# Kernel tuning notes

Measured on AMD Instinct MI355X. Metric: run time of the kernel, lower is better.

## Reference

```python
import jax, jax.numpy as jnp
import numpy as np


def setup_inputs() -> dict:
    key = jax.random.key(0)
    ks = jax.random.split(key, 8)
    B, L, K = 32, 1024, 256
    s = lambda k, shape, sc: jax.random.normal(k, shape, dtype=jnp.float32) * sc
    return {
        "x": s(ks[0], (B, L, K), 1.0),
        "rWx": s(ks[1], (K, 4 * K), 0.05),   # reader LSTM kernel
        "rWh": s(ks[2], (K, 4 * K), 0.05),   # reader recurrent kernel
        "rb": jnp.zeros((4 * K,), jnp.float32),
        "wWx": s(ks[3], (2 * K, 4 * K), 0.05),  # writer LSTM kernel (input dim 2K)
        "wWh": s(ks[4], (K, 4 * K), 0.05),
        "wb": jnp.zeros((4 * K,), jnp.float32),
        "cW": s(ks[5], (2 * K, 2 * K), 0.05),    # composer Dense(2K), linear activation
        "cb": jnp.zeros((2 * K,), jnp.float32),
    }


def _lstm(x_t, h, c, Wx, Wh, b):
    # Keras LSTM: gate order i, f, g(candidate), o; sigmoid recurrent activation, tanh activation
    gates = x_t @ Wx + h @ Wh + b
    i, f, g, o = jnp.split(gates, 4, axis=-1)
    c_new = jax.nn.sigmoid(f) * c + jax.nn.sigmoid(i) * jnp.tanh(g)
    h_new = jax.nn.sigmoid(o) * jnp.tanh(c_new)
    return h_new, c_new


def reference(x, rWx, rWh, rb, wWx, wWh, wb, cW, cb):
    B, L, K = x.shape
    zeros = jnp.zeros((B, K), x.dtype)
    # mem_0 = input (get_initial_state copies input to mem_0); LSTM states start at zero
    carry0 = (zeros, zeros, x, zeros, zeros)  # (hr, cr, mem, hw, cw)

    def step(carry, x_t):
        hr, cr, mem, hw, cw = carry
        # Eq 1: reader LSTM -> o_t
        hr, cr = _lstm(x_t, hr, cr, rWx, rWh, rb)  # o_t = hr, (B, K)
        # Eq 2-3: attention over memory
        z_t = jax.nn.softmax(jnp.einsum('bk,blk->bl', hr, mem), axis=-1)  # (B, L)
        m_rt = jnp.einsum('bl,blk->bk', z_t, mem)                          # (B, K)
        # Eq 4: composer (linear Dense on concat)
        c_t = jnp.concatenate([hr, m_rt], axis=-1) @ cW + cb               # (B, 2K)
        # Eq 5: writer LSTM -> h_t
        hw, cw = _lstm(c_t, hw, cw, wWx, wWh, wb)                          # (B, K)
        # Eq 6: memory update (selective forget + add)
        mem = mem * (1.0 - z_t[..., None]) + hw[:, None, :] * z_t[..., None]
        return (hr, cr, mem, hw, cw), hw

    _, hs = jax.lax.scan(step, carry0, jnp.swapaxes(x, 0, 1))
    # return_mode='all_outputs': full sequence of writer outputs
    return jnp.swapaxes(hs, 0, 1)  # (B, L, K)
```

## Files before the change

kernel.cpp:

```cpp
#include <hip/hip_runtime.h>
#include <math.h>


#define Bb 32
#define LL 1024
#define KK 256
#define ASCOPE __HIP_MEMORY_SCOPE_AGENT
#define FSTR 16

__device__ __forceinline__ float sigf(float v) { return 1.0f / (1.0f + __expf(-v)); }

__device__ __forceinline__ void st_coh2(float* p, float a, float b) {
    float2 v = make_float2(a, b);
    __hip_atomic_store((unsigned long long*)p,
                       __builtin_bit_cast(unsigned long long, v),
                       __ATOMIC_RELAXED, ASCOPE);
}
__device__ __forceinline__ float2 ld_coh2(const float* p) {
    unsigned long long u = __hip_atomic_load((const unsigned long long*)p,
                                             __ATOMIC_RELAXED, ASCOPE);
    return __builtin_bit_cast(float2, u);
}

__device__ __forceinline__ void bar_arrive(unsigned* fown, unsigned val) {
    asm volatile("s_waitcnt vmcnt(0) lgkmcnt(0)" ::: "memory");
    __syncthreads();
    if (threadIdx.x == 0)
        __hip_atomic_store(fown, val, __ATOMIC_RELAXED, ASCOPE);
}
__device__ __forceinline__ void bar_wait(unsigned* fbase, unsigned val) {
    if (threadIdx.x < 64) {
        for (;;) {
            unsigned v = __hip_atomic_load(fbase + threadIdx.x * FSTR,
                                           __ATOMIC_RELAXED, ASCOPE);
            if (__all(v >= val)) break;
            __builtin_amdgcn_s_sleep(1);
        }
    }
    asm volatile("" ::: "memory");
    __syncthreads();
}

__global__ __launch_bounds__(256) void k_pre(
    const float* __restrict__ cW, const float* __restrict__ cb,
    const float* __restrict__ wWx, const float* __restrict__ wb,
    const float* __restrict__ rWx, const float* __restrict__ rWh,
    const float* __restrict__ wWh,
    float* __restrict__ WfT, float* __restrict__ rWT, float* __restrict__ bfv,
    unsigned* __restrict__ flg) {
    int bid = blockIdx.x, tid = threadIdx.x;
    if (bid < 512) {
        __shared__ float srow[512];
        srow[tid] = cW[(size_t)bid * 512 + tid];
        srow[256 + tid] = cW[(size_t)bid * 512 + 256 + tid];
        __syncthreads();
#pragma unroll
        for (int rep = 0; rep < 4; rep++) {
            int col = rep * 256 + tid;
            float a = 0.f;
#pragma unroll 4
            for (int c = 0; c < 512; c++) a += srow[c] * wWx[(size_t)c * 1024 + col];
            WfT[(size_t)col * 768 + bid] = a;
        }
    } else if (bid < 516) {
        int col = (bid - 512) * 256 + tid;
        float a = wb[col];
#pragma unroll 4
        for (int c = 0; c < 512; c++) a += cb[c] * wWx[(size_t)c * 1024 + col];
        bfv[col] = a;
    } else if (bid < 644) {
        int k0 = (bid - 516) * 2;
        for (int kk = k0; kk < k0 + 2; kk++)
            for (int col = tid; col < 1024; col += 256)
                rWT[(size_t)col * 512 + kk] = rWx[(size_t)kk * 1024 + col];
    } else if (bid < 772) {
        int k0 = (bid - 644) * 2;
        for (int kk = k0; kk < k0 + 2; kk++)
            for (int col = tid; col < 1024; col += 256)
                rWT[(size_t)col * 512 + 256 + kk] = rWh[(size_t)kk * 1024 + col];
    } else if (bid < 900) {
        int k0 = (bid - 772) * 2;
        for (int kk = k0; kk < k0 + 2; kk++)
            for (int col = tid; col < 1024; col += 256)
                WfT[(size_t)col * 768 + 512 + kk] = wWh[(size_t)kk * 1024 + col];
    } else {
        int idx = (bid - 900) * 256 + tid;
        flg[idx] = 0u;
    }
}

__global__ __launch_bounds__(512, 1) void k_nse(
    const float* __restrict__ x, const float* __restrict__ rb,
    const float* __restrict__ rWT, const float* __restrict__ WfT,
    const float* __restrict__ bfv, float* __restrict__ st,
    float* __restrict__ out, unsigned* __restrict__ flg) {
    __shared__ float smem[32768 + 6144 + 160];
    float* memT   = smem;
    float* arena  = smem + 32768;
    float* sMw    = smem + 32768 + 6144;
    float* sSw    = sMw + 8;
    float* sMS    = sSw + 8;
    float* sScore = sMS + 16;

    float* hrb[2] = { st, st + 8192 };
    float* hwb[2] = { st + 16384, st + 24576 };
    float* partMS = st + 32832;
    float* partV  = st + 33344;

    int g = blockIdx.x, tid = threadIdx.x;
    int w = tid >> 6, ln = tid & 63;
    int bA = g >> 3;
    int bg = g >> 6, gl = g & 63;
    int j0 = gl * 4;
    int wstar = gl >> 3;
    unsigned* fA = flg + (bg * 64) * FSTR;
    unsigned* fB = flg + (256 + bg * 64) * FSTR;
    unsigned* fAo = fA + gl * FSTR;
    unsigned* fBo = fB + gl * FSTR;

    int ks = ln & 3, jq = (ln >> 2) & 3, gate = ln >> 4;
    int col = gate * KK + j0 + jq;
    int jl = ln & 3;
    int bw = bg * 8 + w;
    float* shb = arena + w * 768;
    float* sT  = arena + w * 640;

    const float4* wfc = (const float4*)(WfT + (size_t)col * 768);
    const float4* rwc = (const float4*)(rWT + (size_t)col * 512);
    float4 w2[16];
#pragma unroll
    for (int i = 0; i < 16; i++) w2[i] = wfc[64 + i * 4 + ks];
    float4 rw1[8];
#pragma unroll
    for (int i = 0; i < 8; i++) rw1[i] = rwc[i * 4 + ks];

    float crreg = 0.f, cwreg = 0.f;

    const float4* xsrc = (const float4*)(x + ((size_t)bA * LL + (size_t)(g & 7) * 128) * KK);
#pragma unroll
    for (int i = 0; i < 16; i++) ((float4*)memT)[tid + i * 512] = xsrc[tid + i * 512];
    {
        ((float4*)shb)[ln] = ((const float4*)(x + (size_t)bw * LL * KK))[ln];
        ((float4*)(shb + 256))[ln] = make_float4(0.f, 0.f, 0.f, 0.f);
        float racc = (ks == 0) ? rb[col] : 0.f;
        const float4* ip = (const float4*)shb;
#pragma unroll
        for (int i = 0; i < 8; i++) {
            float4 a = ip[i * 4 + ks];
            racc += a.x * rw1[i].x + a.y * rw1[i].y + a.z * rw1[i].z + a.w * rw1[i].w;
        }
#pragma unroll 8
        for (int i = 8; i < 32; i++) {
            int idx = i * 4 + ks;
            float4 a = ip[idx], q = rwc[idx];
            racc += a.x * q.x + a.y * q.y + a.z * q.z + a.w * q.w;
        }
        racc += __shfl_xor(racc, 1);
        racc += __shfl_xor(racc, 2);
        float gi = __shfl(racc, 4 * jl), gG = __shfl(racc, 32 + 4 * jl);
        float go = __shfl(racc, 48 + 4 * jl);
        float cn = sigf(gi) * tanhf(gG);
        float hn = sigf(go) * tanhf(cn);
        crreg = cn;
        float pa = __shfl(hn, 2 * (ln & 31)), pb = __shfl(hn, 2 * (ln & 31) + 1);
        if (ln < 2) st_coh2(hrb[0] + bw * KK + j0 + 2 * ln, pa, pb);
    }
    bar_arrive(fBo, 1u);
    float4 xreg = ((const float4*)(x + ((size_t)bw * LL + 1) * KK))[ln];
    bar_wait(fB, 1u);

    for (int t = 0; t < LL; t++) {
        int cur = t & 1, prv = cur ^ 1;
        const float* hp = hrb[cur] + bA * KK + ln * 4;
        float2 ha = ld_coh2(hp), hc = ld_coh2(hp + 2);
        float4 h4 = make_float4(ha.x, ha.y, hc.x, hc.y);
        float4 hrs2, hws2, w4 = make_float4(0.f, 0.f, 0.f, 0.f);
        {
            const float* hq = hrb[cur] + bw * KK + ln * 4;
            float2 a = ld_coh2(hq), c = ld_coh2(hq + 2);
            hrs2 = make_float4(a.x, a.y, c.x, c.y);
        }
        float Mprev = 0.f, invS = 0.f;
        if (t > 0) {
            const float* wp0 = hwb[prv] + bA * KK + ln * 4;
            float2 wa = ld_coh2(wp0), wc = ld_coh2(wp0 + 2);
            w4 = make_float4(wa.x, wa.y, wc.x, wc.y);
            const float* hq = hwb[prv] + bw * KK + ln * 4;
            float2 a = ld_coh2(hq), c = ld_coh2(hq + 2);
            hws2 = make_float4(a.x, a.y, c.x, c.y);
            Mprev = sMS[wstar * 2];
            invS = 1.0f / sMS[wstar * 2 + 1];
        } else {
            hws2 = make_float4(0.f, 0.f, 0.f, 0.f);
        }
        float dp[16];
        float* rowp = memT + w * 16 * KK;
        if (t > 0) {
            float scs[16];
            {
                const float4* sp = (const float4*)(sScore + w * 16);
#pragma unroll
                for (int q2 = 0; q2 < 4; q2++) {
                    float4 s4 = sp[q2];
                    scs[q2 * 4 + 0] = s4.x; scs[q2 * 4 + 1] = s4.y;
                    scs[q2 * 4 + 2] = s4.z; scs[q2 * 4 + 3] = s4.w;
                }
            }
#pragma unroll
            for (int i = 0; i < 16; i++) {
                float4* vp = (float4*)(rowp + i * KK) + ln;
                float4 v = *vp;
                float z = __expf(scs[i] - Mprev) * invS;
                float om = 1.0f - z;
                v.x = v.x * om + w4.x * z;
                v.y = v.y * om + w4.y * z;
                v.z = v.z * om + w4.z * z;
                v.w = v.w * om + w4.w * z;
                *vp = v;
                dp[i] = h4.x * v.x + h4.y * v.y + h4.z * v.z + h4.w * v.w;
            }
        } else {
#pragma unroll
            for (int i = 0; i < 16; i++) {
                float4 v = *((float4*)(rowp + i * KK) + ln);
                dp[i] = h4.x * v.x + h4.y * v.y + h4.z * v.z + h4.w * v.w;
            }
        }
        {
            int rr = ln >> 3, kk2 = ln & 7;
#pragma unroll
            for (int hh = 0; hh < 2; hh++) {
                int o = hh * 8;
                *(float2*)(sT + ln * 10 + 0) = make_float2(dp[o + 0], dp[o + 1]);
                *(float2*)(sT + ln * 10 + 2) = make_float2(dp[o + 2], dp[o + 3]);
                *(float2*)(sT + ln * 10 + 4) = make_float2(dp[o + 4], dp[o + 5]);
                *(float2*)(sT + ln * 10 + 6) = make_float2(dp[o + 6], dp[o + 7]);
                float ps = 0.f;
#pragma unroll
                for (int j = 0; j < 8; j++) ps += sT[(j * 8 + kk2) * 10 + rr];
                ps += __shfl_xor(ps, 1);
                ps += __shfl_xor(ps, 2);
                ps += __shfl_xor(ps, 4);
                if (kk2 == 0) sScore[w * 16 + o + rr] = ps;
            }
        }
        {
            float scs2[16];
            const float4* sp = (const float4*)(sScore + w * 16);
#pragma unroll
            for (int q2 = 0; q2 < 4; q2++) {
                float4 s4 = sp[q2];
                scs2[q2 * 4 + 0] = s4.x; scs2[q2 * 4 + 1] = s4.y;
                scs2[q2 * 4 + 2] = s4.z; scs2[q2 * 4 + 3] = s4.w;
            }
            float M16 = scs2[0];
#pragma unroll
            for (int i = 1; i < 16; i++) M16 = fmaxf(M16, scs2[i]);
            float Sw = 0.f;
            float4 Vw = make_float4(0.f, 0.f, 0.f, 0.f);
#pragma unroll
            for (int i = 0; i < 16; i++) {
                float e = __expf(scs2[i] - M16);
                Sw += e;
                float4 v = *((float4*)(rowp + i * KK) + ln);
                Vw.x += e * v.x; Vw.y += e * v.y; Vw.z += e * v.z; Vw.w += e * v.w;
            }
            ((float4*)(arena + w * 640))[ln] = Vw;
            if (ln == 0) { sMw[w] = M16; sSw[w] = Sw; }
        }
        __syncthreads();
        if (tid < 128) {
            float M = sMw[0];
#pragma unroll
            for (int q2 = 1; q2 < 8; q2++) M = fmaxf(M, sMw[q2]);
            float S = 0.f, V0 = 0.f, V1 = 0.f;
#pragma unroll
            for (int q2 = 0; q2 < 8; q2++) {
                float e = __expf(sMw[q2] - M);
                S += e * sSw[q2];
                V0 += e * arena[q2 * 640 + 2 * tid];
                V1 += e * arena[q2 * 640 + 2 * tid + 1];
            }
            st_coh2(partV + (size_t)g * KK + 2 * tid, V0, V1);
            if (tid == 0) st_coh2(partMS + g * 2, M, S);
        }
        bar_arrive(fAo, (unsigned)(t + 1));

        if (t + 1 < LL) ((float4*)shb)[ln] = xreg;
        ((float4*)(shb + 256))[ln] = hrs2;
        ((float4*)(shb + 512))[ln] = hws2;

        {
            unsigned tgt = (unsigned)(t + 1);
            for (;;) {
                unsigned v = tgt;
                if (ln < 8)
                    v = __hip_atomic_load(fA + (8 * w + ln) * FSTR, __ATOMIC_RELAXED, ASCOPE);
                if (__all(v >= tgt)) break;
                __builtin_amdgcn_s_sleep(1);
            }
        }
        float2 pms[8], pva[8], pvb[8];
#pragma unroll
        for (int q2 = 0; q2 < 8; q2++) {
            pms[q2] = ld_coh2(partMS + (bw * 8 + q2) * 2);
            const float* pv = partV + (size_t)(bw * 8 + q2) * KK + ln * 4;
            pva[q2] = ld_coh2(pv);
            pvb[q2] = ld_coh2(pv + 2);
        }
        float gpre;
        {
            float acc = (ks == 0) ? bfv[col] : 0.f;
            const float4* ip1 = (const float4*)(shb + 256);
            const float4* ip2 = (const float4*)(shb + 512);
#pragma unroll 8
            for (int i = 0; i < 16; i++) {
                int idx = i * 4 + ks;
                float4 a = ip1[idx], q = wfc[idx];
                acc += a.x * q.x + a.y * q.y + a.z * q.z + a.w * q.w;
            }
#pragma unroll 8
            for (int i = 0; i < 16; i++) {
                int idx = i * 4 + ks;
                float4 a = ip2[idx], q = wfc[128 + idx];
                acc += a.x * q.x + a.y * q.y + a.z * q.z + a.w * q.w;
            }
            gpre = acc;
        }
        if (t + 1 < LL) {
            float racc = (ks == 0) ? rb[col] : 0.f;
            const float4* ip = (const float4*)shb;
#pragma unroll
            for (int i = 0; i < 8; i++) {
                float4 a = ip[i * 4 + ks];
                racc += a.x * rw1[i].x + a.y * rw1[i].y + a.z * rw1[i].z + a.w * rw1[i].w;
            }
#pragma unroll 8
            for (int i = 8; i < 32; i++) {
                int idx = i * 4 + ks;
                float4 a = ip[idx], q = rwc[idx];
                racc += a.x * q.x + a.y * q.y + a.z * q.z + a.w * q.w;
            }
            racc += __shfl_xor(racc, 1);
            racc += __shfl_xor(racc, 2);
            float gi = __shfl(racc, 4 * jl), gf = __shfl(racc, 16 + 4 * jl);
            float gG = __shfl(racc, 32 + 4 * jl), go = __shfl(racc, 48 + 4 * jl);
            float cn = sigf(gf) * crreg + sigf(gi) * tanhf(gG);
            float hn = sigf(go) * tanhf(cn);
            crreg = cn;
            float pa = __shfl(hn, 2 * (ln & 31)), pb = __shfl(hn, 2 * (ln & 31) + 1);
            if (ln < 2) st_coh2(hrb[prv] + bw * KK + j0 + 2 * ln, pa, pb);
        }
        {
            float M = pms[0].x;
#pragma unroll
            for (int q2 = 1; q2 < 8; q2++) M = fmaxf(M, pms[q2].x);
            float S = 0.f;
            float4 V = make_float4(0.f, 0.f, 0.f, 0.f);
#pragma unroll
            for (int q2 = 0; q2 < 8; q2++) {
                float e = __expf(pms[q2].x - M);
                S += e * pms[q2].y;
                V.x += e * pva[q2].x; V.y += e * pva[q2].y;
                V.z += e * pvb[q2].x; V.w += e * pvb[q2].y;
            }
            float rS = 1.0f / S;
            ((float4*)shb)[ln] = make_float4(V.x * rS, V.y * rS, V.z * rS, V.w * rS);
            if (ln == 0) { sMS[w * 2] = M; sMS[w * 2 + 1] = S; }
            float acc = gpre;
            const float4* ip = (const float4*)shb;
#pragma unroll
            for (int i = 0; i < 16; i++) {
                float4 a = ip[i * 4 + ks];
                acc += a.x * w2[i].x + a.y * w2[i].y + a.z * w2[i].z + a.w * w2[i].w;
            }
            acc += __shfl_xor(acc, 1);
            acc += __shfl_xor(acc, 2);
            float gi = __shfl(acc, 4 * jl), gf = __shfl(acc, 16 + 4 * jl);
            float gG = __shfl(acc, 32 + 4 * jl), go = __shfl(acc, 48 + 4 * jl);
            float cp = (t > 0) ? cwreg : 0.f;
            float cn = sigf(gf) * cp + sigf(gi) * tanhf(gG);
            float hn = sigf(go) * tanhf(cn);
            cwreg = cn;
            float pa = __shfl(hn, 2 * (ln & 31)), pb = __shfl(hn, 2 * (ln & 31) + 1);
            if (ln < 2) {
                st_coh2(hwb[cur] + bw * KK + j0 + 2 * ln, pa, pb);
                *(float2*)(out + ((size_t)bw * LL + t) * KK + j0 + 2 * ln) =
                    make_float2(pa, pb);
            }
        }
        bar_arrive(fBo, (unsigned)(t + 2));
        if (t + 2 < LL)
            xreg = ((const float4*)(x + ((size_t)bw * LL + (size_t)(t + 2)) * KK))[ln];
        bar_wait(fB, (unsigned)(t + 2));
    }
}

extern "C" void kernel_launch(void* const* d_in, const int* in_sizes, int n_in,
                              void* d_out, int out_size, void* d_ws, size_t ws_size,
                              hipStream_t stream) {
    const float* x   = (const float*)d_in[0];
    const float* rWx = (const float*)d_in[1];
    const float* rWh = (const float*)d_in[2];
    const float* rb  = (const float*)d_in[3];
    const float* wWx = (const float*)d_in[4];
    const float* wWh = (const float*)d_in[5];
    const float* wb  = (const float*)d_in[6];
    const float* cW  = (const float*)d_in[7];
    const float* cb  = (const float*)d_in[8];
    float* out = (float*)d_out;

    float* ws = (float*)d_ws;
    float* WfT = ws;
    float* rWT = ws + 786432;
    float* bfv = ws + 786432 + 524288;
    float* st  = bfv + 1024;
    unsigned* flg = (unsigned*)(st + 98880);

    k_pre<<<932, 256, 0, stream>>>(cW, cb, wWx, wb, rWx, rWh, wWh, WfT, rWT, bfv, flg);

    const float* a_x = x; const float* a_rb = rb;
    const float* a_rWT = rWT; const float* a_WfT = WfT; const float* a_bf = bfv;
    float* a_st = st; float* a_out = out; unsigned* a_flg = flg;
    void* args[] = { &a_x, &a_rb, &a_rWT, &a_WfT, &a_bf, &a_st, &a_out, &a_flg };
    hipLaunchCooperativeKernel(reinterpret_cast<void*>(k_nse), dim3(256), dim3(512),
                               args, 0, stream);
}
```

Measured before the change: 15.01 ms.

## Share LSTM gate weights across batch rows by re-partitioning gate GEMV work

Before, each wavefront computed all 16 gate columns for one batch row, so every wave re-read the same weight columns. Now each wavefront owns two gate columns and computes them for all 8 batch rows of the group, reading inputs from a block-wide shared arena. Partial sums go through shared memory, and 32 threads then apply the LSTM cell nonlinearities. This cuts redundant weight traffic and register pressure (the rw1 cache is dropped), at the cost of extra __syncthreads per step. The arena stride is padded to 776 and the transpose scratch stride to 9, with staggered read offsets, to reduce LDS bank conflicts.

```diff
diff --git a/kernel.cpp b/kernel.cpp
--- a/kernel.cpp
+++ b/kernel.cpp
@@ -5,6 +5,7 @@
 #define Bb 32
 #define LL 1024
 #define KK 256
+#define AR 776
 #define ASCOPE __HIP_MEMORY_SCOPE_AGENT
 #define FSTR 16
 
@@ -94,13 +95,15 @@
     const float* __restrict__ rWT, const float* __restrict__ WfT,
     const float* __restrict__ bfv, float* __restrict__ st,
     float* __restrict__ out, unsigned* __restrict__ flg) {
-    __shared__ float smem[32768 + 6144 + 160];
+    __shared__ float smem[32768 + 8 * AR + 8 + 8 + 16 + 128 + 128 + 128];
     float* memT   = smem;
     float* arena  = smem + 32768;
-    float* sMw    = smem + 32768 + 6144;
+    float* sMw    = arena + 8 * AR;
     float* sSw    = sMw + 8;
     float* sMS    = sSw + 8;
     float* sScore = sMS + 16;
+    float* sGr    = sScore + 128;
+    float* sGw    = sGr + 128;
 
     float* hrb[2] = { st, st + 8192 };
     float* hwb[2] = { st + 16384, st + 24576 };
@@ -112,61 +115,58 @@
     int bA = g >> 3;
     int bg = g >> 6, gl = g & 63;
     int j0 = gl * 4;
-    int wstar = gl >> 3;
     unsigned* fA = flg + (bg * 64) * FSTR;
     unsigned* fB = flg + (256 + bg * 64) * FSTR;
     unsigned* fAo = fA + gl * FSTR;
     unsigned* fBo = fB + gl * FSTR;
 
-    int ks = ln & 3, jq = (ln >> 2) & 3, gate = ln >> 4;
-    int col = gate * KK + j0 + jq;
-    int jl = ln & 3;
-    int bw = bg * 8 + w;
-    float* shb = arena + w * 768;
-    float* sT  = arena + w * 640;
+    int bln = ln & 7, ks = (ln >> 3) & 3, cp = ln >> 5;
+    int c = 2 * w + cp;
+    int gate = c >> 2, jlc = c & 3;
+    int col = gate * KK + j0 + jlc;
+    int bglw = bg * 8 + w;
 
     const float4* wfc = (const float4*)(WfT + (size_t)col * 768);
     const float4* rwc = (const float4*)(rWT + (size_t)col * 512);
     float4 w2[16];
 #pragma unroll
-    for (int i = 0; i < 16; i++) w2[i] = wfc[64 + i * 4 + ks];
-    float4 rw1[8];
-#pragma unroll
-    for (int i = 0; i < 8; i++) rw1[i] = rwc[i * 4 + ks];
+    for (int i = 0; i < 16; i++) w2[i] = wfc[64 + ks * 16 + ((i + 3 * ks) & 15)];
 
     float crreg = 0.f, cwreg = 0.f;
 
     const float4* xsrc = (const float4*)(x + ((size_t)bA * LL + (size_t)(g & 7) * 128) * KK);
 #pragma unroll
     for (int i = 0; i < 16; i++) ((float4*)memT)[tid + i * 512] = xsrc[tid + i * 512];
+    ((float4*)(arena + w * AR))[ln] = ((const float4*)(x + (size_t)bglw * LL * KK))[ln];
+    ((float4*)(arena + w * AR + 256))[ln] = make_float4(0.f, 0.f, 0.f, 0.f);
+    __syncthreads();
     {
-        ((float4*)shb)[ln] = ((const float4*)(x + (size_t)bw * LL * KK))[ln];
-        ((float4*)(shb + 256))[ln] = make_float4(0.f, 0.f, 0.f, 0.f);
-        float racc = (ks == 0) ? rb[col] : 0.f;
-        const float4* ip = (const float4*)shb;
-#pragma unroll
-        for (int i = 0; i < 8; i++) {
-            float4 a = ip[i * 4 + ks];
-            racc += a.x * rw1[i].x + a.y * rw1[i].y + a.z * rw1[i].z + a.w * rw1[i].w;
-        }
+        float accr = 0.f;
+        const float4* ain = (const float4*)(arena + bln * AR);
 #pragma unroll 8
-        for (int i = 8; i < 32; i++) {
-            int idx = i * 4 + ks;
-            float4 a = ip[idx], q = rwc[idx];
-            racc += a.x * q.x + a.y * q.y + a.z * q.z + a.w * q.w;
-        }
-        racc += __shfl_xor(racc, 1);
-        racc += __shfl_xor(racc, 2);
-        float gi = __shfl(racc, 4 * jl), gG = __shfl(racc, 32 + 4 * jl);
-        float go = __shfl(racc, 48 + 4 * jl);
+        for (int i = 0; i < 32; i++) {
+            int idx = ks * 32 + ((i + 5 * ks) & 31);
+            float4 a = ain[idx], q = rwc[idx];
+            accr += a.x * q.x + a.y * q.y + a.z * q.z + a.w * q.w;
+        }
+        accr += __shfl_xor(accr, 8);
+        accr += __shfl_xor(accr, 16);
+        if (!(ln & 24)) sGr[c * 8 + bln] = accr + rb[col];
+    }
+    __syncthreads();
+    if (tid < 32) {
+        int pb = tid & 7, pj = tid >> 3;
+        int bgp = bg * 8 + pb;
+        float gi = sGr[(0 + pj) * 8 + pb], gG = sGr[(8 + pj) * 8 + pb];
+        float go = sGr[(12 + pj) * 8 + pb];
         float cn = sigf(gi) * tanhf(gG);
         float hn = sigf(go) * tanhf(cn);
         crreg = cn;
-        float pa = __shfl(hn, 2 * (ln & 31)), pb = __shfl(hn, 2 * (ln & 31) + 1);
-        if (ln < 2) st_coh2(hrb[0] + bw * KK + j0 + 2 * ln, pa, pb);
+        float hn2 = __shfl(hn, tid + 8);
+        if (!(pj & 1)) st_coh2(hrb[0] + bgp * KK + j0 + pj, hn, hn2);
     }
     bar_arrive(fBo, 1u);
-    float4 xreg = ((const float4*)(x + ((size_t)bw * LL + 1) * KK))[ln];
+    float4 xreg = ((const float4*)(x + ((size_t)bglw * LL + 1) * KK))[ln];
     bar_wait(fB, 1u);
 
     for (int t = 0; t < LL; t++) {
@@ -176,20 +176,20 @@
         float4 h4 = make_float4(ha.x, ha.y, hc.x, hc.y);
         float4 hrs2, hws2, w4 = make_float4(0.f, 0.f, 0.f, 0.f);
         {
-            const float* hq = hrb[cur] + bw * KK + ln * 4;
-            float2 a = ld_coh2(hq), c = ld_coh2(hq + 2);
-            hrs2 = make_float4(a.x, a.y, c.x, c.y);
+            const float* hq = hrb[cur] + bglw * KK + ln * 4;
+            float2 a = ld_coh2(hq), cc = ld_coh2(hq + 2);
+            hrs2 = make_float4(a.x, a.y, cc.x, cc.y);
         }
         float Mprev = 0.f, invS = 0.f;
         if (t > 0) {
             const float* wp0 = hwb[prv] + bA * KK + ln * 4;
             float2 wa = ld_coh2(wp0), wc = ld_coh2(wp0 + 2);
             w4 = make_float4(wa.x, wa.y, wc.x, wc.y);
-            const float* hq = hwb[prv] + bw * KK + ln * 4;
-            float2 a = ld_coh2(hq), c = ld_coh2(hq + 2);
-            hws2 = make_float4(a.x, a.y, c.x, c.y);
-            Mprev = sMS[wstar * 2];
-            invS = 1.0f / sMS[wstar * 2 + 1];
+            const float* hq = hwb[prv] + bglw * KK + ln * 4;
+            float2 a = ld_coh2(hq), cc = ld_coh2(hq + 2);
+            hws2 = make_float4(a.x, a.y, cc.x, cc.y);
+            Mprev = sMS[(bA & 7) * 2];
+            invS = 1.0f / sMS[(bA & 7) * 2 + 1];
         } else {
             hws2 = make_float4(0.f, 0.f, 0.f, 0.f);
         }
@@ -197,14 +197,12 @@
         float* rowp = memT + w * 16 * KK;
         if (t > 0) {
             float scs[16];
-            {
-                const float4* sp = (const float4*)(sScore + w * 16);
-#pragma unroll
-                for (int q2 = 0; q2 < 4; q2++) {
-                    float4 s4 = sp[q2];
-                    scs[q2 * 4 + 0] = s4.x; scs[q2 * 4 + 1] = s4.y;
-                    scs[q2 * 4 + 2] = s4.z; scs[q2 * 4 + 3] = s4.w;
-                }
+            const float4* sp = (const float4*)(sScore + w * 16);
+#pragma unroll
+            for (int q2 = 0; q2 < 4; q2++) {
+                float4 s4 = sp[q2];
+                scs[q2 * 4 + 0] = s4.x; scs[q2 * 4 + 1] = s4.y;
+                scs[q2 * 4 + 2] = s4.z; scs[q2 * 4 + 3] = s4.w;
             }
 #pragma unroll
             for (int i = 0; i < 16; i++) {
@@ -227,17 +225,16 @@
             }
         }
         {
+            float* sT = arena + w * AR;
             int rr = ln >> 3, kk2 = ln & 7;
 #pragma unroll
             for (int hh = 0; hh < 2; hh++) {
                 int o = hh * 8;
-                *(float2*)(sT + ln * 10 + 0) = make_float2(dp[o + 0], dp[o + 1]);
-                *(float2*)(sT + ln * 10 + 2) = make_float2(dp[o + 2], dp[o + 3]);
-                *(float2*)(sT + ln * 10 + 4) = make_float2(dp[o + 4], dp[o + 5]);
-                *(float2*)(sT + ln * 10 + 6) = make_float2(dp[o + 6], dp[o + 7]);
+#pragma unroll
+                for (int j = 0; j < 8; j++) sT[ln * 9 + j] = dp[o + j];
                 float ps = 0.f;
 #pragma unroll
-                for (int j = 0; j < 8; j++) ps += sT[(j * 8 + kk2) * 10 + rr];
+                for (int j = 0; j < 8; j++) ps += sT[(j * 8 + kk2) * 9 + rr];
                 ps += __shfl_xor(ps, 1);
                 ps += __shfl_xor(ps, 2);
                 ps += __shfl_xor(ps, 4);
@@ -265,7 +262,7 @@
                 float4 v = *((float4*)(rowp + i * KK) + ln);
                 Vw.x += e * v.x; Vw.y += e * v.y; Vw.z += e * v.z; Vw.w += e * v.w;
             }
-            ((float4*)(arena + w * 640))[ln] = Vw;
+            ((float4*)(arena + w * AR))[ln] = Vw;
             if (ln == 0) { sMw[w] = M16; sSw[w] = Sw; }
         }
         __syncthreads();
@@ -278,17 +275,49 @@
             for (int q2 = 0; q2 < 8; q2++) {
                 float e = __expf(sMw[q2] - M);
                 S += e * sSw[q2];
-                V0 += e * arena[q2 * 640 + 2 * tid];
-                V1 += e * arena[q2 * 640 + 2 * tid + 1];
+                V0 += e * arena[q2 * AR + 2 * tid];
+                V1 += e * arena[q2 * AR + 2 * tid + 1];
             }
             st_coh2(partV + (size_t)g * KK + 2 * tid, V0, V1);
             if (tid == 0) st_coh2(partMS + g * 2, M, S);
         }
         bar_arrive(fAo, (unsigned)(t + 1));
 
-        if (t + 1 < LL) ((float4*)shb)[ln] = xreg;
-        ((float4*)(shb + 256))[ln] = hrs2;
-        ((float4*)(shb + 512))[ln] = hws2;
+        if (t + 1 < LL) ((float4*)(arena + w * AR))[ln] = xreg;
+        ((float4*)(arena + w * AR + 256))[ln] = hrs2;
+        ((float4*)(arena + w * AR + 512))[ln] = hws2;
+        __syncthreads();
+
+        float accw = (ks == 0) ? bfv[col] : 0.f;
+        {
+            const float4* ain = (const float4*)(arena + bln * AR);
+#pragma unroll 8
+            for (int i = 0; i < 16; i++) {
+                int idx = ks * 16 + ((i + 3 * ks) & 15);
+                float4 a = ain[64 + idx], q = wfc[idx];
+                accw += a.x * q.x + a.y * q.y + a.z * q.z + a.w * q.w;
+            }
+#pragma unroll 8
+            for (int i = 0; i < 16; i++) {
+                int idx = ks * 16 + ((i + 3 * ks) & 15);
+                float4 a = ain[128 + idx], q = wfc[128 + idx];
+                accw += a.x * q.x + a.y * q.y + a.z * q.z + a.w * q.w;
+            }
+        }
+        if (t + 1 < LL) {
+            float accr = 0.f;
+            const float4* ain = (const float4*)(arena + bln * AR);
+#pragma unroll 8
+            for (int i = 0; i < 32; i++) {
+                int idx = ks * 32 + ((i + 5 * ks) & 31);
+                float4 a = ain[idx], q = rwc[idx];
+                accr += a.x * q.x + a.y * q.y + a.z * q.z + a.w * q.w;
+            }
+            accr += __shfl_xor(accr, 8);
+            accr += __shfl_xor(accr, 16);
+            if (!(ln & 24)) sGr[c * 8 + bln] = accr + rb[col];
+        }
+        __syncthreads();
 
         {
             unsigned tgt = (unsigned)(t + 1);
@@ -300,58 +329,17 @@
                 __builtin_amdgcn_s_sleep(1);
             }
         }
-        float2 pms[8], pva[8], pvb[8];
-#pragma unroll
-        for (int q2 = 0; q2 < 8; q2++) {
-            pms[q2] = ld_coh2(partMS + (bw * 8 + q2) * 2);
-            const float* pv = partV + (size_t)(bw * 8 + q2) * KK + ln * 4;
-            pva[q2] = ld_coh2(pv);
-            pvb[q2] = ld_coh2(pv + 2);
-        }
-        float gpre;
-        {
-            float acc = (ks == 0) ? bfv[col] : 0.f;
-            const float4* ip1 = (const float4*)(shb + 256);
-            const float4* ip2 = (const float4*)(shb + 512);
-#pragma unroll 8
-            for (int i = 0; i < 16; i++) {
-                int idx = i * 4 + ks;
-                float4 a = ip1[idx], q = wfc[idx];
-                acc += a.x * q.x + a.y * q.y + a.z * q.z + a.w * q.w;
-            }
-#pragma unroll 8
-            for (int i = 0; i < 16; i++) {
-                int idx = i * 4 + ks;
-                float4 a = ip2[idx], q = wfc[128 + idx];
-                acc += a.x * q.x + a.y * q.y + a.z * q.z + a.w * q.w;
-            }
-            gpre = acc;
-        }
-        if (t + 1 < LL) {
-            float racc = (ks == 0) ? rb[col] : 0.f;
-            const float4* ip = (const float4*)shb;
-#pragma unroll
-            for (int i = 0; i < 8; i++) {
-                float4 a = ip[i * 4 + ks];
-                racc += a.x * rw1[i].x + a.y * rw1[i].y + a.z * rw1[i].z + a.w * rw1[i].w;
-            }
-#pragma unroll 8
-            for (int i = 8; i < 32; i++) {
-                int idx = i * 4 + ks;
-                float4 a = ip[idx], q = rwc[idx];
-                racc += a.x * q.x + a.y * q.y + a.z * q.z + a.w * q.w;
-            }
-            racc += __shfl_xor(racc, 1);
-            racc += __shfl_xor(racc, 2);
-            float gi = __shfl(racc, 4 * jl), gf = __shfl(racc, 16 + 4 * jl);
-            float gG = __shfl(racc, 32 + 4 * jl), go = __shfl(racc, 48 + 4 * jl);
-            float cn = sigf(gf) * crreg + sigf(gi) * tanhf(gG);
-            float hn = sigf(go) * tanhf(cn);
-            crreg = cn;
-            float pa = __shfl(hn, 2 * (ln & 31)), pb = __shfl(hn, 2 * (ln & 31) + 1);
-            if (ln < 2) st_coh2(hrb[prv] + bw * KK + j0 + 2 * ln, pa, pb);
-        }
-        {
+        {
+            float2 pms[8];
+            float2 pva[8], pvb[8];
+#pragma unroll
+            for (int q2 = 0; q2 < 8; q2++) {
+                int src = bg * 64 + w * 8 + q2;
+                pms[q2] = ld_coh2(partMS + src * 2);
+                const float* pv = partV + (size_t)src * KK + ln * 4;
+                pva[q2] = ld_coh2(pv);
+                pvb[q2] = ld_coh2(pv + 2);
+            }
             float M = pms[0].x;
 #pragma unroll
             for (int q2 = 1; q2 < 8; q2++) M = fmaxf(M, pms[q2].x);
@@ -365,33 +353,56 @@
                 V.z += e * pvb[q2].x; V.w += e * pvb[q2].y;
             }
             float rS = 1.0f / S;
-            ((float4*)shb)[ln] = make_float4(V.x * rS, V.y * rS, V.z * rS, V.w * rS);
+            ((float4*)(arena + w * AR))[ln] =
+                make_float4(V.x * rS, V.y * rS, V.z * rS, V.w * rS);
             if (ln == 0) { sMS[w * 2] = M; sMS[w * 2 + 1] = S; }
-            float acc = gpre;
-            const float4* ip = (const float4*)shb;
-#pragma unroll
-            for (int i = 0; i < 16; i++) {
-                float4 a = ip[i * 4 + ks];
-                acc += a.x * w2[i].x + a.y * w2[i].y + a.z * w2[i].z + a.w * w2[i].w;
-            }
-            acc += __shfl_xor(acc, 1);
-            acc += __shfl_xor(acc, 2);
-            float gi = __shfl(acc, 4 * jl), gf = __shfl(acc, 16 + 4 * jl);
-            float gG = __shfl(acc, 32 + 4 * jl), go = __shfl(acc, 48 + 4 * jl);
-            float cp = (t > 0) ? cwreg : 0.f;
-            float cn = sigf(gf) * cp + sigf(gi) * tanhf(gG);
-            float hn = sigf(go) * tanhf(cn);
-            cwreg = cn;
-            float pa = __shfl(hn, 2 * (ln & 31)), pb = __shfl(hn, 2 * (ln & 31) + 1);
-            if (ln < 2) {
-                st_coh2(hwb[cur] + bw * KK + j0 + 2 * ln, pa, pb);
-                *(float2*)(out + ((size_t)bw * LL + t) * KK + j0 + 2 * ln) =
-                    make_float2(pa, pb);
+        }
+        __syncthreads();
+
+        {
+            const float4* ain = (const float4*)(arena + bln * AR);
+#pragma unroll
+            for (int i = 0; i < 16; i++) {
+                int idx = ks * 16 + ((i + 3 * ks) & 15);
+                float4 a = ain[idx];
+                accw += a.x * w2[i].x + a.y * w2[i].y + a.z * w2[i].z + a.w * w2[i].w;
+            }
+            accw += __shfl_xor(accw, 8);
+            accw += __shfl_xor(accw, 16);
+            if (!(ln & 24)) sGw[c * 8 + bln] = accw;
+        }
+        __syncthreads();
+
+        if (tid < 32) {
+            int pb = tid & 7, pj = tid >> 3;
+            int bgp = bg * 8 + pb;
+            if (t + 1 < LL) {
+                float gi = sGr[(0 + pj) * 8 + pb], gf = sGr[(4 + pj) * 8 + pb];
+                float gG = sGr[(8 + pj) * 8 + pb], go = sGr[(12 + pj) * 8 + pb];
+                float cn = sigf(gf) * crreg + sigf(gi) * tanhf(gG);
+                float hn = sigf(go) * tanhf(cn);
+                crreg = cn;
+                float hn2 = __shfl(hn, tid + 8);
+                if (!(pj & 1)) st_coh2(hrb[prv] + bgp * KK + j0 + pj, hn, hn2);
+            }
+            {
+                float gi = sGw[(0 + pj) * 8 + pb], gf = sGw[(4 + pj) * 8 + pb];
+                float gG = sGw[(8 + pj) * 8 + pb], go = sGw[(12 + pj) * 8 + pb];
+                float cp2 = (t > 0) ? cwreg : 0.f;
+                float cn = sigf(gf) * cp2 + sigf(gi) * tanhf(gG);
+                float hn = sigf(go) * tanhf(cn);
+                cwreg = cn;
+                float hn2 = __shfl(hn, tid + 8);
+                if (!(pj & 1)) {
+                    st_coh2(hwb[cur] + bgp * KK + j0 + pj, hn, hn2);
+                    *(float2*)(out + ((size_t)bgp * LL + t) * KK + j0 + pj) =
+                        make_float2(hn, hn2);
+                }
             }
         }
         bar_arrive(fBo, (unsigned)(t + 2));
         if (t + 2 < LL)
-            xreg = ((const float4*)(x + ((size_t)bw * LL + (size_t)(t + 2)) * KK))[ln];
+            xreg = ((const float4*)(x + ((size_t)bglw * LL + (size_t)(t + 2)) * KK))[ln];
         bar_wait(fB, (unsigned)(t + 2));
     }
 }
```

Result: faster. 13.15 ms (-12.4%).
